# Optimization experiments

Measured on AMD Instinct MI355X. Metric: run time of the kernel, lower is better.

The kernel has to match this reference:

```python
import jax, jax.numpy as jnp
import numpy as np

B, N, D, H, O, K, N_USER, C = 1, 4096, 64, 4, 64, 2, 4000, 2


def setup_inputs() -> dict:
    key = jax.random.key(0)
    ks = jax.random.split(key, 7)
    h = jax.random.normal(ks[0], (B, N, D), jnp.float32)
    # dense 0/1 adjacency per heterogeneous kind, with self-loops so no row is empty
    adj = jax.random.randint(ks[1], (K, B, N, N), 0, 2).astype(jnp.float32)
    hadj = jnp.maximum(adj, jnp.eye(N, dtype=jnp.float32))
    s = 1.0 / np.sqrt(D).astype(np.float32)
    w = jax.random.normal(ks[2], (K, H, D, O), jnp.float32) * s
    a_src = jax.random.normal(ks[3], (K, H, O, 1), jnp.float32) * (1.0 / np.sqrt(O).astype(np.float32))
    a_dst = jax.random.normal(ks[4], (K, H, O, 1), jnp.float32) * (1.0 / np.sqrt(O).astype(np.float32))
    fc_w = jax.random.normal(ks[5], (C, O * K), jnp.float32) * (1.0 / np.sqrt(O * K).astype(np.float32))
    fc_b = jnp.zeros((C,), jnp.float32)
    return {"h": h, "hadj": hadj, "w": w, "a_src": a_src, "a_dst": a_dst, "fc_w": fc_w, "fc_b": fc_b}


def _gat(h, adj, w_k, a_src_k, a_dst_k):
    # h: (B,N,D); adj: (B,N,N); w_k: (H,D,O); a_*: (H,O,1)
    h_prime = jnp.einsum('bnf,hfo->bhno', h, w_k)          # (B,H,N,O)
    t = jnp.tanh(h_prime)
    attn_src = jnp.einsum('bhno,hoi->bhni', t, a_src_k)    # (B,H,N,1)
    attn_dst = jnp.einsum('bhno,hoi->bhni', t, a_dst_k)    # (B,H,N,1)
    attn = attn_src + jnp.swapaxes(attn_dst, -1, -2)       # (B,H,N,N) broadcast add
    attn = jnp.where(attn >= 0, attn, 0.2 * attn)          # LeakyReLU(0.2)
    attn = jnp.where(adj[:, None] > 0, attn, -jnp.inf)     # dense mask
    attn = jax.nn.softmax(attn, axis=-1)                   # dropout is a no-op in eval
    out = jnp.einsum('bhnm,bhmo->bhno', attn, h_prime)     # (B,H,N,O)
    return out.mean(axis=1)                                # mean over heads -> (B,N,O)


def reference(h, hadj, w, a_src, a_dst, fc_w, fc_b):
    embs = []
    for k in range(K):  # small fixed loop over heterogeneous node kinds
        x = _gat(h, hadj[k], w[k], a_src[k], a_dst[k])
        embs.append(x[:, :N_USER])
    type_aware = jnp.concatenate(embs, axis=-1)            # (B, N_USER, K*O)
    logits = type_aware @ fc_w.T + fc_b                    # (B, N_USER, C)
    return jax.nn.log_softmax(logits, axis=-1)
```

## Files before the change

### kernel.cpp

```cpp
#include <hip/hip_runtime.h>
#include <math.h>

constexpr int KK = 2;
constexpr int HH = 4;
constexpr int NN = 4096;
constexpr int DD = 64;
constexpr int OO = 64;
constexpr int NU = 4000;
constexpr int CC = 2;
constexpr float LOG2E = 1.44269504088896340736f;

__device__ __forceinline__ float fexp2(float x) {
#if __has_builtin(__builtin_amdgcn_exp2f)
  return __builtin_amdgcn_exp2f(x);
#else
  return exp2f(x);
#endif
}
__device__ __forceinline__ float frcp(float x) {
#if __has_builtin(__builtin_amdgcn_rcpf)
  return __builtin_amdgcn_rcpf(x);
#else
  return 1.0f / x;
#endif
}
__device__ __forceinline__ float ftanh(float x) {
  float e = fexp2(x * (2.0f * LOG2E));
  return 1.0f - 2.0f * frcp(e + 1.0f);
}

__global__ __launch_bounds__(128) void gat_phase1(
    const float* __restrict__ hsrc, const float* __restrict__ w,
    const float* __restrict__ a_src, const float* __restrict__ a_dst,
    const float* __restrict__ fc_w,
    float* __restrict__ src_s, float4* __restrict__ att) {
  const int kh = blockIdx.y;
  const int k = kh >> 2;
  const int i0 = blockIdx.x * 128;
  const int tid = threadIdx.x;

  __shared__ float w_s[DD * OO];
  __shared__ float h_s[DD][128];
  __shared__ float asrc_s[OO], adst_s[OO], fw0[OO], fw1[OO];
  __shared__ float redl[4][32][17];

  const float* wp = w + (size_t)kh * DD * OO;
  for (int t = tid; t < DD * OO; t += 128) w_s[t] = wp[t];
  if (tid < OO) {
    asrc_s[tid] = a_src[kh * OO + tid];
    adst_s[tid] = a_dst[kh * OO + tid];
    fw0[tid] = fc_w[0 * (KK * OO) + k * OO + tid];
    fw1[tid] = fc_w[1 * (KK * OO) + k * OO + tid];
  }
  {
    const float* hr = hsrc + (size_t)(i0 + tid) * DD;
#pragma unroll
    for (int f4 = 0; f4 < DD; f4 += 4) {
      float4 v = *(const float4*)(hr + f4);
      h_s[f4 + 0][tid] = v.x;
      h_s[f4 + 1][tid] = v.y;
      h_s[f4 + 2][tid] = v.z;
      h_s[f4 + 3][tid] = v.w;
    }
  }
  __syncthreads();

  const int og = tid >> 5;
  const int rg = tid & 31;
  const int o0 = og * 16;
  const int r0 = rg * 4;

  float hp[4][16];
#pragma unroll
  for (int r = 0; r < 4; ++r)
#pragma unroll
    for (int o = 0; o < 16; ++o) hp[r][o] = 0.0f;

#pragma unroll 4
  for (int f = 0; f < DD; ++f) {
    float hr0 = h_s[f][r0 + 0];
    float hr1 = h_s[f][r0 + 1];
    float hr2 = h_s[f][r0 + 2];
    float hr3 = h_s[f][r0 + 3];
#pragma unroll
    for (int o = 0; o < 16; ++o) {
      float wv = w_s[f * OO + o0 + o];
      hp[0][o] = fmaf(hr0, wv, hp[0][o]);
      hp[1][o] = fmaf(hr1, wv, hp[1][o]);
      hp[2][o] = fmaf(hr2, wv, hp[2][o]);
      hp[3][o] = fmaf(hr3, wv, hp[3][o]);
    }
  }

#pragma unroll
  for (int r = 0; r < 4; ++r) {
    float sp = 0.0f, dp = 0.0f, g0 = 0.0f, g1 = 0.0f;
#pragma unroll
    for (int o = 0; o < 16; ++o) {
      float v = hp[r][o];
      float t = ftanh(v);
      sp = fmaf(t, asrc_s[o0 + o], sp);
      dp = fmaf(t, adst_s[o0 + o], dp);
      g0 = fmaf(v, fw0[o0 + o], g0);
      g1 = fmaf(v, fw1[o0 + o], g1);
    }
    redl[og][rg][r * 4 + 0] = sp;
    redl[og][rg][r * 4 + 1] = dp;
    redl[og][rg][r * 4 + 2] = g0;
    redl[og][rg][r * 4 + 3] = g1;
  }
  __syncthreads();

  {
    const int lr = tid;
    const int rrg = lr >> 2, rr = lr & 3;
    float sp = 0.0f, dp = 0.0f, g0 = 0.0f, g1 = 0.0f;
#pragma unroll
    for (int q = 0; q < 4; ++q) {
      sp += redl[q][rrg][rr * 4 + 0];
      dp += redl[q][rrg][rr * 4 + 1];
      g0 += redl[q][rrg][rr * 4 + 2];
      g1 += redl[q][rrg][rr * 4 + 3];
    }
    const int i = i0 + lr;
    src_s[kh * NN + i] = sp * LOG2E;
    att[(size_t)kh * NN + i] = make_float4(dp * LOG2E, g0, g1, 0.0f);
  }
}

__global__ __launch_bounds__(128) void gat_phase2(
    const float* __restrict__ adj, const float* __restrict__ src_s,
    const float4* __restrict__ att, float* __restrict__ S) {
  const int k = blockIdx.y;
  const int i0 = blockIdx.x * 8;
  const int tid = threadIdx.x;
  const int lane = tid & 63;
  const int wv = tid >> 6;

  float srcv[8][4];
#pragma unroll
  for (int r = 0; r < 8; ++r)
#pragma unroll
    for (int q = 0; q < 4; ++q)
      srcv[r][q] = src_s[(k * HH + q) * NN + i0 + r];

  float lacc[8][4];
  float cacc[8][4][2];
#pragma unroll
  for (int r = 0; r < 8; ++r)
#pragma unroll
    for (int q = 0; q < 4; ++q) {
      lacc[r][q] = 0.0f;
      cacc[r][q][0] = 0.0f;
      cacc[r][q][1] = 0.0f;
    }

  const float* adjk = adj + (size_t)k * NN * NN;
  const float4* attk = att + (size_t)k * HH * NN;

  for (int jb = tid * 4; jb < NN; jb += 512) {
    float4 aj[8];
#pragma unroll
    for (int r = 0; r < 8; ++r)
      aj[r] = *(const float4*)(adjk + (size_t)(i0 + r) * NN + jb);
#pragma unroll
    for (int jj = 0; jj < 4; ++jj) {
      float4 av[4];
      av[0] = attk[0 * NN + jb + jj];
      av[1] = attk[1 * NN + jb + jj];
      av[2] = attk[2 * NN + jb + jj];
      av[3] = attk[3 * NN + jb + jj];
#pragma unroll
      for (int r = 0; r < 8; ++r) {
        const float a = (jj == 0) ? aj[r].x
                      : (jj == 1) ? aj[r].y
                      : (jj == 2) ? aj[r].z
                                  : aj[r].w;
#pragma unroll
        for (int q = 0; q < 4; ++q) {
          float s = srcv[r][q] + av[q].x;
          float sl = fmaxf(s, 0.2f * s);
          float p = a * fexp2(sl);
          lacc[r][q] += p;
          cacc[r][q][0] = fmaf(p, av[q].y, cacc[r][q][0]);
          cacc[r][q][1] = fmaf(p, av[q].z, cacc[r][q][1]);
        }
      }
    }
  }

#pragma unroll
  for (int r = 0; r < 8; ++r)
#pragma unroll
    for (int q = 0; q < 4; ++q) {
      float x0 = lacc[r][q], x1 = cacc[r][q][0], x2 = cacc[r][q][1];
#pragma unroll
      for (int off = 32; off > 0; off >>= 1) {
        x0 += __shfl_xor(x0, off, 64);
        x1 += __shfl_xor(x1, off, 64);
        x2 += __shfl_xor(x2, off, 64);
      }
      lacc[r][q] = x0;
      cacc[r][q][0] = x1;
      cacc[r][q][1] = x2;
    }

  __shared__ float red2[2][96];
  if (lane == 0) {
#pragma unroll
    for (int r = 0; r < 8; ++r)
#pragma unroll
      for (int q = 0; q < 4; ++q) {
        red2[wv][(r * 4 + q) * 3 + 0] = lacc[r][q];
        red2[wv][(r * 4 + q) * 3 + 1] = cacc[r][q][0];
        red2[wv][(r * 4 + q) * 3 + 2] = cacc[r][q][1];
      }
  }
  __syncthreads();
  if (tid < 16) {
    const int r = tid >> 1, c = tid & 1;
    float sum = 0.0f;
#pragma unroll
    for (int q = 0; q < 4; ++q) {
      float lsum = red2[0][(r * 4 + q) * 3 + 0] + red2[1][(r * 4 + q) * 3 + 0];
      float asum = red2[0][(r * 4 + q) * 3 + 1 + c] + red2[1][(r * 4 + q) * 3 + 1 + c];
      sum += asum / lsum;
    }
    S[((size_t)k * NU + i0 + r) * CC + c] = 0.25f * sum;
  }
}

__global__ __launch_bounds__(256) void gat_phase3(
    const float* __restrict__ S, const float* __restrict__ fc_b,
    float* __restrict__ out) {
  const int i = blockIdx.x * 256 + threadIdx.x;
  if (i >= NU) return;
  float l0 = S[(size_t)(0 * NU + i) * CC + 0] + S[((size_t)NU + i) * CC + 0] + fc_b[0];
  float l1 = S[(size_t)(0 * NU + i) * CC + 1] + S[((size_t)NU + i) * CC + 1] + fc_b[1];
  float m = fmaxf(l0, l1);
  float lse = m + logf(expf(l0 - m) + expf(l1 - m));
  out[i * CC + 0] = l0 - lse;
  out[i * CC + 1] = l1 - lse;
}

extern "C" void kernel_launch(void* const* d_in, const int* in_sizes, int n_in,
                              void* d_out, int out_size, void* d_ws, size_t ws_size,
                              hipStream_t stream) {
  const float* hsrc  = (const float*)d_in[0];
  const float* hadj  = (const float*)d_in[1];
  const float* w     = (const float*)d_in[2];
  const float* a_src = (const float*)d_in[3];
  const float* a_dst = (const float*)d_in[4];
  const float* fc_w  = (const float*)d_in[5];
  const float* fc_b  = (const float*)d_in[6];
  float* out = (float*)d_out;

  char* ws = (char*)d_ws;
  float*  src_s = (float*)ws;
  float4* att   = (float4*)(ws + 131072);
  float*  S     = (float*)(ws + 131072 + 524288);

  dim3 g1(NN / 128, KK * HH);
  gat_phase1<<<g1, 128, 0, stream>>>(hsrc, w, a_src, a_dst, fc_w, src_s, att);
  dim3 g2(NU / 8, KK);
  gat_phase2<<<g2, 128, 0, stream>>>(hadj, src_s, att, S);
  gat_phase3<<<(NU + 255) / 256, 256, 0, stream>>>(S, fc_b, out);
}
```

Before: 263.1 us.

## Split attention columns across blocks and reorganize phase1/phase2 work layout

Phase2 now splits the neighbor dimension into four chunks per kind, with each wave handling two rows over a contiguous chunk. Partial softmax sums go to a workspace buffer that phase3 reduces. The att layout becomes node-major with heads interleaved, so one node's four head float4s are contiguous. Phase1 is retiled to 64 rows with 256 threads, vectorized LDS reads and shuffle reductions. The goal is more blocks and parallelism on the memory-bound adjacency stream, at the cost of a larger partial-sum buffer and an extra reduction step.

```diff
diff --git a/kernel.cpp b/kernel.cpp
--- a/kernel.cpp
+++ b/kernel.cpp
@@ -8,6 +8,8 @@
 constexpr int OO = 64;
 constexpr int NU = 4000;
 constexpr int CC = 2;
+constexpr int JSPLIT = 4;
+constexpr int JCHUNK = NN / JSPLIT;
 constexpr float LOG2E = 1.44269504088896340736f;
 
 __device__ __forceinline__ float fexp2(float x) {
@@ -29,125 +31,127 @@
   return 1.0f - 2.0f * frcp(e + 1.0f);
 }
 
-__global__ __launch_bounds__(128) void gat_phase1(
+__global__ __launch_bounds__(256) void gat_phase1(
     const float* __restrict__ hsrc, const float* __restrict__ w,
     const float* __restrict__ a_src, const float* __restrict__ a_dst,
     const float* __restrict__ fc_w,
     float* __restrict__ src_s, float4* __restrict__ att) {
   const int kh = blockIdx.y;
   const int k = kh >> 2;
-  const int i0 = blockIdx.x * 128;
+  const int i0 = blockIdx.x * 64;
   const int tid = threadIdx.x;
 
-  __shared__ float w_s[DD * OO];
-  __shared__ float h_s[DD][128];
-  __shared__ float asrc_s[OO], adst_s[OO], fw0[OO], fw1[OO];
-  __shared__ float redl[4][32][17];
-
-  const float* wp = w + (size_t)kh * DD * OO;
-  for (int t = tid; t < DD * OO; t += 128) w_s[t] = wp[t];
-  if (tid < OO) {
-    asrc_s[tid] = a_src[kh * OO + tid];
-    adst_s[tid] = a_dst[kh * OO + tid];
-    fw0[tid] = fc_w[0 * (KK * OO) + k * OO + tid];
-    fw1[tid] = fc_w[1 * (KK * OO) + k * OO + tid];
-  }
+  __shared__ float h_s[DD][68];
+  __shared__ float w_s[DD][OO];
+
   {
-    const float* hr = hsrc + (size_t)(i0 + tid) * DD;
-#pragma unroll
-    for (int f4 = 0; f4 < DD; f4 += 4) {
-      float4 v = *(const float4*)(hr + f4);
-      h_s[f4 + 0][tid] = v.x;
-      h_s[f4 + 1][tid] = v.y;
-      h_s[f4 + 2][tid] = v.z;
-      h_s[f4 + 3][tid] = v.w;
-    }
+    const float4* wp = (const float4*)(w + (size_t)kh * DD * OO);
+    float4* ws4 = (float4*)w_s;
+    for (int t = tid; t < DD * OO / 4; t += 256) ws4[t] = wp[t];
+  }
+  for (int t = tid; t < 1024; t += 256) {
+    const int row = t >> 4;
+    const int f4 = (t & 15) * 4;
+    float4 v = *(const float4*)(hsrc + (size_t)(i0 + row) * DD + f4);
+    h_s[f4 + 0][row] = v.x;
+    h_s[f4 + 1][row] = v.y;
+    h_s[f4 + 2][row] = v.z;
+    h_s[f4 + 3][row] = v.w;
   }
   __syncthreads();
 
-  const int og = tid >> 5;
-  const int rg = tid & 31;
-  const int o0 = og * 16;
+  const int og = tid & 15;
+  const int rg = tid >> 4;
+  const int o0 = og * 4;
   const int r0 = rg * 4;
 
-  float hp[4][16];
-#pragma unroll
-  for (int r = 0; r < 4; ++r)
-#pragma unroll
-    for (int o = 0; o < 16; ++o) hp[r][o] = 0.0f;
-
-#pragma unroll 4
+  float hp[4][4];
+#pragma unroll
+  for (int j = 0; j < 4; ++j)
+#pragma unroll
+    for (int u = 0; u < 4; ++u) hp[j][u] = 0.0f;
+
+#pragma unroll 8
   for (int f = 0; f < DD; ++f) {
-    float hr0 = h_s[f][r0 + 0];
-    float hr1 = h_s[f][r0 + 1];
-    float hr2 = h_s[f][r0 + 2];
-    float hr3 = h_s[f][r0 + 3];
-#pragma unroll
-    for (int o = 0; o < 16; ++o) {
-      float wv = w_s[f * OO + o0 + o];
-      hp[0][o] = fmaf(hr0, wv, hp[0][o]);
-      hp[1][o] = fmaf(hr1, wv, hp[1][o]);
-      hp[2][o] = fmaf(hr2, wv, hp[2][o]);
-      hp[3][o] = fmaf(hr3, wv, hp[3][o]);
-    }
-  }
-
-#pragma unroll
-  for (int r = 0; r < 4; ++r) {
+    float4 hv = *(const float4*)&h_s[f][r0];
+    float4 wv = *(const float4*)&w_s[f][o0];
+    hp[0][0] = fmaf(hv.x, wv.x, hp[0][0]);
+    hp[0][1] = fmaf(hv.x, wv.y, hp[0][1]);
+    hp[0][2] = fmaf(hv.x, wv.z, hp[0][2]);
+    hp[0][3] = fmaf(hv.x, wv.w, hp[0][3]);
+    hp[1][0] = fmaf(hv.y, wv.x, hp[1][0]);
+    hp[1][1] = fmaf(hv.y, wv.y, hp[1][1]);
+    hp[1][2] = fmaf(hv.y, wv.z, hp[1][2]);
+    hp[1][3] = fmaf(hv.y, wv.w, hp[1][3]);
+    hp[2][0] = fmaf(hv.z, wv.x, hp[2][0]);
+    hp[2][1] = fmaf(hv.z, wv.y, hp[2][1]);
+    hp[2][2] = fmaf(hv.z, wv.z, hp[2][2]);
+    hp[2][3] = fmaf(hv.z, wv.w, hp[2][3]);
+    hp[3][0] = fmaf(hv.w, wv.x, hp[3][0]);
+    hp[3][1] = fmaf(hv.w, wv.y, hp[3][1]);
+    hp[3][2] = fmaf(hv.w, wv.z, hp[3][2]);
+    hp[3][3] = fmaf(hv.w, wv.w, hp[3][3]);
+  }
+
+  float as[4], ad[4], f0[4], f1[4];
+#pragma unroll
+  for (int u = 0; u < 4; ++u) {
+    as[u] = a_src[kh * OO + o0 + u];
+    ad[u] = a_dst[kh * OO + o0 + u];
+    f0[u] = fc_w[0 * (KK * OO) + k * OO + o0 + u];
+    f1[u] = fc_w[1 * (KK * OO) + k * OO + o0 + u];
+  }
+
+#pragma unroll
+  for (int j = 0; j < 4; ++j) {
     float sp = 0.0f, dp = 0.0f, g0 = 0.0f, g1 = 0.0f;
 #pragma unroll
-    for (int o = 0; o < 16; ++o) {
-      float v = hp[r][o];
+    for (int u = 0; u < 4; ++u) {
+      float v = hp[j][u];
       float t = ftanh(v);
-      sp = fmaf(t, asrc_s[o0 + o], sp);
-      dp = fmaf(t, adst_s[o0 + o], dp);
-      g0 = fmaf(v, fw0[o0 + o], g0);
-      g1 = fmaf(v, fw1[o0 + o], g1);
-    }
-    redl[og][rg][r * 4 + 0] = sp;
-    redl[og][rg][r * 4 + 1] = dp;
-    redl[og][rg][r * 4 + 2] = g0;
-    redl[og][rg][r * 4 + 3] = g1;
-  }
-  __syncthreads();
-
-  {
-    const int lr = tid;
-    const int rrg = lr >> 2, rr = lr & 3;
-    float sp = 0.0f, dp = 0.0f, g0 = 0.0f, g1 = 0.0f;
-#pragma unroll
-    for (int q = 0; q < 4; ++q) {
-      sp += redl[q][rrg][rr * 4 + 0];
-      dp += redl[q][rrg][rr * 4 + 1];
-      g0 += redl[q][rrg][rr * 4 + 2];
-      g1 += redl[q][rrg][rr * 4 + 3];
-    }
-    const int i = i0 + lr;
-    src_s[kh * NN + i] = sp * LOG2E;
-    att[(size_t)kh * NN + i] = make_float4(dp * LOG2E, g0, g1, 0.0f);
-  }
-}
-
-__global__ __launch_bounds__(128) void gat_phase2(
+      sp = fmaf(t, as[u], sp);
+      dp = fmaf(t, ad[u], dp);
+      g0 = fmaf(v, f0[u], g0);
+      g1 = fmaf(v, f1[u], g1);
+    }
+#pragma unroll
+    for (int off = 1; off < 16; off <<= 1) {
+      sp += __shfl_xor(sp, off, 64);
+      dp += __shfl_xor(dp, off, 64);
+      g0 += __shfl_xor(g0, off, 64);
+      g1 += __shfl_xor(g1, off, 64);
+    }
+    if (og == 0) {
+      const int i = i0 + r0 + j;
+      src_s[kh * NN + i] = sp * LOG2E;
+      att[((size_t)k * NN + i) * HH + (kh & 3)] =
+          make_float4(dp * LOG2E, g0, g1, 0.0f);
+    }
+  }
+}
+
+__global__ __launch_bounds__(256) void gat_phase2(
     const float* __restrict__ adj, const float* __restrict__ src_s,
-    const float4* __restrict__ att, float* __restrict__ S) {
-  const int k = blockIdx.y;
+    const float4* __restrict__ att, float* __restrict__ P) {
+  const int k = blockIdx.y >> 2;
+  const int chunk = blockIdx.y & 3;
   const int i0 = blockIdx.x * 8;
   const int tid = threadIdx.x;
+  const int wv = tid >> 6;
   const int lane = tid & 63;
-  const int wv = tid >> 6;
-
-  float srcv[8][4];
-#pragma unroll
-  for (int r = 0; r < 8; ++r)
+  const int r0 = i0 + wv * 2;
+
+  float srcv[2][4];
+#pragma unroll
+  for (int r = 0; r < 2; ++r)
 #pragma unroll
     for (int q = 0; q < 4; ++q)
-      srcv[r][q] = src_s[(k * HH + q) * NN + i0 + r];
-
-  float lacc[8][4];
-  float cacc[8][4][2];
-#pragma unroll
-  for (int r = 0; r < 8; ++r)
+      srcv[r][q] = src_s[(k * HH + q) * NN + r0 + r];
+
+  float lacc[2][4];
+  float cacc[2][4][2];
+#pragma unroll
+  for (int r = 0; r < 2; ++r)
 #pragma unroll
     for (int q = 0; q < 4; ++q) {
       lacc[r][q] = 0.0f;
@@ -156,41 +160,49 @@
     }
 
   const float* adjk = adj + (size_t)k * NN * NN;
-  const float4* attk = att + (size_t)k * HH * NN;
-
-  for (int jb = tid * 4; jb < NN; jb += 512) {
-    float4 aj[8];
-#pragma unroll
-    for (int r = 0; r < 8; ++r)
-      aj[r] = *(const float4*)(adjk + (size_t)(i0 + r) * NN + jb);
+  const float4* attk = att + (size_t)k * NN * HH;
+  const int jb0 = chunk * JCHUNK + lane * 4;
+
+#pragma unroll 2
+  for (int it = 0; it < JCHUNK / 256; ++it) {
+    const int jb = jb0 + it * 256;
+    float4 ar0 = *(const float4*)(adjk + (size_t)(r0 + 0) * NN + jb);
+    float4 ar1 = *(const float4*)(adjk + (size_t)(r0 + 1) * NN + jb);
+    float e0[4] = {ar0.x, ar0.y, ar0.z, ar0.w};
+    float e1[4] = {ar1.x, ar1.y, ar1.z, ar1.w};
+    const float4* attb = attk + (size_t)jb * HH;
 #pragma unroll
     for (int jj = 0; jj < 4; ++jj) {
       float4 av[4];
-      av[0] = attk[0 * NN + jb + jj];
-      av[1] = attk[1 * NN + jb + jj];
-      av[2] = attk[2 * NN + jb + jj];
-      av[3] = attk[3 * NN + jb + jj];
-#pragma unroll
-      for (int r = 0; r < 8; ++r) {
-        const float a = (jj == 0) ? aj[r].x
-                      : (jj == 1) ? aj[r].y
-                      : (jj == 2) ? aj[r].z
-                                  : aj[r].w;
-#pragma unroll
-        for (int q = 0; q < 4; ++q) {
-          float s = srcv[r][q] + av[q].x;
+      av[0] = attb[jj * HH + 0];
+      av[1] = attb[jj * HH + 1];
+      av[2] = attb[jj * HH + 2];
+      av[3] = attb[jj * HH + 3];
+#pragma unroll
+      for (int q = 0; q < 4; ++q) {
+        const float d = av[q].x, g0 = av[q].y, g1 = av[q].z;
+        {
+          float s = srcv[0][q] + d;
           float sl = fmaxf(s, 0.2f * s);
-          float p = a * fexp2(sl);
-          lacc[r][q] += p;
-          cacc[r][q][0] = fmaf(p, av[q].y, cacc[r][q][0]);
-          cacc[r][q][1] = fmaf(p, av[q].z, cacc[r][q][1]);
+          float p = e0[jj] * fexp2(sl);
+          lacc[0][q] += p;
+          cacc[0][q][0] = fmaf(p, g0, cacc[0][q][0]);
+          cacc[0][q][1] = fmaf(p, g1, cacc[0][q][1]);
         }
-      }
-    }
-  }
-
-#pragma unroll
-  for (int r = 0; r < 8; ++r)
+        {
+          float s = srcv[1][q] + d;
+          float sl = fmaxf(s, 0.2f * s);
+          float p = e1[jj] * fexp2(sl);
+          lacc[1][q] += p;
+          cacc[1][q][0] = fmaf(p, g0, cacc[1][q][0]);
+          cacc[1][q][1] = fmaf(p, g1, cacc[1][q][1]);
+        }
+      }
+    }
+  }
+
+#pragma unroll
+  for (int r = 0; r < 2; ++r)
 #pragma unroll
     for (int q = 0; q < 4; ++q) {
       float x0 = lacc[r][q], x1 = cacc[r][q][0], x2 = cacc[r][q][1];
@@ -205,38 +217,43 @@
       cacc[r][q][1] = x2;
     }
 
-  __shared__ float red2[2][96];
   if (lane == 0) {
 #pragma unroll
-    for (int r = 0; r < 8; ++r)
+    for (int r = 0; r < 2; ++r)
 #pragma unroll
       for (int q = 0; q < 4; ++q) {
-        red2[wv][(r * 4 + q) * 3 + 0] = lacc[r][q];
-        red2[wv][(r * 4 + q) * 3 + 1] = cacc[r][q][0];
-        red2[wv][(r * 4 + q) * 3 + 2] = cacc[r][q][1];
-      }
-  }
-  __syncthreads();
-  if (tid < 16) {
-    const int r = tid >> 1, c = tid & 1;
-    float sum = 0.0f;
-#pragma unroll
-    for (int q = 0; q < 4; ++q) {
-      float lsum = red2[0][(r * 4 + q) * 3 + 0] + red2[1][(r * 4 + q) * 3 + 0];
-      float asum = red2[0][(r * 4 + q) * 3 + 1 + c] + red2[1][(r * 4 + q) * 3 + 1 + c];
-      sum += asum / lsum;
-    }
-    S[((size_t)k * NU + i0 + r) * CC + c] = 0.25f * sum;
+        size_t base =
+            (((size_t)(k * JSPLIT + chunk) * HH + q) * 3) * NU + (r0 + r);
+        P[base] = lacc[r][q];
+        P[base + NU] = cacc[r][q][0];
+        P[base + 2 * (size_t)NU] = cacc[r][q][1];
+      }
   }
 }
 
 __global__ __launch_bounds__(256) void gat_phase3(
-    const float* __restrict__ S, const float* __restrict__ fc_b,
+    const float* __restrict__ P, const float* __restrict__ fc_b,
     float* __restrict__ out) {
   const int i = blockIdx.x * 256 + threadIdx.x;
   if (i >= NU) return;
-  float l0 = S[(size_t)(0 * NU + i) * CC + 0] + S[((size_t)NU + i) * CC + 0] + fc_b[0];
-  float l1 = S[(size_t)(0 * NU + i) * CC + 1] + S[((size_t)NU + i) * CC + 1] + fc_b[1];
+  float l0 = fc_b[0], l1 = fc_b[1];
+#pragma unroll
+  for (int k = 0; k < KK; ++k) {
+#pragma unroll
+    for (int q = 0; q < HH; ++q) {
+      float ls = 0.0f, a0 = 0.0f, a1 = 0.0f;
+#pragma unroll
+      for (int ch = 0; ch < JSPLIT; ++ch) {
+        size_t b = (((size_t)(k * JSPLIT + ch) * HH + q) * 3) * NU + i;
+        ls += P[b];
+        a0 += P[b + NU];
+        a1 += P[b + 2 * (size_t)NU];
+      }
+      float inv = 1.0f / ls;
+      l0 = fmaf(0.25f * a0, inv, l0);
+      l1 = fmaf(0.25f * a1, inv, l1);
+    }
+  }
   float m = fmaxf(l0, l1);
   float lse = m + logf(expf(l0 - m) + expf(l1 - m));
   out[i * CC + 0] = l0 - lse;
@@ -258,11 +275,11 @@
   char* ws = (char*)d_ws;
   float*  src_s = (float*)ws;
   float4* att   = (float4*)(ws + 131072);
-  float*  S     = (float*)(ws + 131072 + 524288);
-
-  dim3 g1(NN / 128, KK * HH);
-  gat_phase1<<<g1, 128, 0, stream>>>(hsrc, w, a_src, a_dst, fc_w, src_s, att);
-  dim3 g2(NU / 8, KK);
-  gat_phase2<<<g2, 128, 0, stream>>>(hadj, src_s, att, S);
-  gat_phase3<<<(NU + 255) / 256, 256, 0, stream>>>(S, fc_b, out);
-}
+  float*  P     = (float*)(ws + 131072 + 524288);
+
+  dim3 g1(NN / 64, KK * HH);
+  gat_phase1<<<g1, 256, 0, stream>>>(hsrc, w, a_src, a_dst, fc_w, src_s, att);
+  dim3 g2(NU / 8, KK * JSPLIT);
+  gat_phase2<<<g2, 256, 0, stream>>>(hadj, src_s, att, P);
+  gat_phase3<<<(NU + 255) / 256, 256, 0, stream>>>(P, fc_b, out);
+}
```

Result: slower. 330.7 us (+25.7%).
